# Kernel optimization log

Hardware: AMD Instinct MI355X
Metric: run time of the kernel (lower is better)

The kernel has to match this reference:

```python
import jax, jax.numpy as jnp
import numpy as np

B, H, D, N, RPE = 4, 8, 64, 4096, 64
GAMMA = 0.999
N_LAYERS = 3
EPS = 1e-5


def _layernorm(x, w, b):
    mu = jnp.mean(x, axis=-1, keepdims=True)
    var = jnp.mean((x - mu) ** 2, axis=-1, keepdims=True)
    return (x - mu) / jnp.sqrt(var + EPS) * w + b


def _rpe(pos, pp_w, pp_b, ln_w, ln_b, lw, lb, oln_w, oln_b, out_w, out_b):
    # pos: [m, 1] scalar relative positions -> [h, m, d] Toeplitz kernel values
    x = pos @ pp_w + pp_b                       # [m, rpe_dim]
    for i in range(N_LAYERS):                   # residual=False path
        x = _layernorm(x, ln_w[i], ln_b[i])
        x = jax.nn.relu(x) @ lw[i] + lb[i]
    x = jax.nn.relu(_layernorm(x, oln_w, oln_b)) @ out_w + out_b  # [m, h*d]
    m = x.shape[0]
    return x.reshape(m, H, D).transpose(1, 0, 2)  # 'n (h d) -> h n d'


def setup_inputs() -> dict:
    key = jax.random.key(0)
    ks = jax.random.split(key, 4)
    x = jax.random.normal(ks[0], (B, H, N, D), dtype=jnp.float32)
    pp_w = jax.random.normal(ks[1], (1, RPE), dtype=jnp.float32) * 0.1
    pp_b = jnp.zeros((RPE,), dtype=jnp.float32)
    ln_w = jnp.ones((N_LAYERS, RPE), dtype=jnp.float32)
    ln_b = jnp.zeros((N_LAYERS, RPE), dtype=jnp.float32)
    lw = jax.random.normal(ks[2], (N_LAYERS, RPE, RPE), dtype=jnp.float32) * 0.1
    lb = jnp.zeros((N_LAYERS, RPE), dtype=jnp.float32)
    oln_w = jnp.ones((RPE,), dtype=jnp.float32)
    oln_b = jnp.zeros((RPE,), dtype=jnp.float32)
    out_w = jax.random.normal(ks[3], (RPE, H * D), dtype=jnp.float32) * 0.1
    out_b = jnp.zeros((H * D,), dtype=jnp.float32)
    return {"x": x, "pp_w": pp_w, "pp_b": pp_b, "ln_w": ln_w, "ln_b": ln_b,
            "lw": lw, "lb": lb, "oln_w": oln_w, "oln_b": oln_b,
            "out_w": out_w, "out_b": out_b}


def reference(x, pp_w, pp_b, ln_w, ln_b, lw, lb, oln_w, oln_b, out_w, out_b):
    # Tno.forward_fft, causal=True, use_decay=True, par_type=1
    rpe_args = (pp_w, pp_b, ln_w, ln_b, lw, lb, oln_w, oln_b, out_w, out_b)
    zero = _rpe(jnp.zeros((1, 1), dtype=x.dtype), *rpe_args)          # [h,1,d]
    pos_idx = jnp.arange(1, N, dtype=x.dtype).reshape(-1, 1)          # [n-1,1]
    pos = _rpe(pos_idx, *rpe_args)                                    # [h,n-1,d]
    coef = jnp.arange(1, N, dtype=x.dtype).reshape(1, -1, 1)
    pos = (GAMMA ** coef) * pos                                       # exp decay
    a = jax.nn.silu(jnp.concatenate([zero, pos, zero], axis=1))       # [h,n+1,d]
    # causal Toeplitz conv via length-2n FFT
    y = jnp.fft.rfft(x, 2 * N, axis=-2)                               # [b,h,n+1,d] cplx
    v = jnp.fft.rfft(a, 2 * N, axis=-2)[None]                         # [1,h,n+1,d]
    out = jnp.fft.irfft(v * y, 2 * N, axis=-2)[:, :, :N, :]
    return out
```

## Files before the change

### kernel.cpp

```cpp
#include <hip/hip_runtime.h>
#include <math.h>

#define NSEQ 4096
#define MFT  4096
#define CHX  2048
#define CHA  512

#define LPAD 4224
static __device__ __forceinline__ int pad(int i) { return i + (i >> 5); }

static __device__ __forceinline__ float wsum64(float v) {
    v += __shfl_xor(v, 1);
    v += __shfl_xor(v, 2);
    v += __shfl_xor(v, 4);
    v += __shfl_xor(v, 8);
    v += __shfl_xor(v, 16);
    v += __shfl_xor(v, 32);
    return v;
}

__global__ __launch_bounds__(256) void k_twiddle(float2* __restrict__ tw) {
    int t = blockIdx.x * 256 + threadIdx.x;
    float fr = (float)t * (2.0f / (float)MFT);
    tw[t] = make_float2(cospif(fr), -sinpif(fr));
}

__global__ __launch_bounds__(256) void k_transpose(const float* __restrict__ src,
                                                   float* __restrict__ dst,
                                                   int R, int C) {
    __shared__ float tile[64][65];
    size_t slab = (size_t)blockIdx.z * (size_t)R * (size_t)C;
    int c0 = blockIdx.x * 64, r0 = blockIdx.y * 64;
    int t = threadIdx.x;
    int tc = t & 63, t4 = t >> 6;
    const float* s = src + slab + (size_t)r0 * C + c0;
#pragma unroll
    for (int k = 0; k < 16; ++k) {
        int rr = t4 + k * 4;
        tile[rr][tc] = s[(size_t)rr * C + tc];
    }
    __syncthreads();
    float* d = dst + slab + (size_t)c0 * R + r0;
#pragma unroll
    for (int k = 0; k < 16; ++k) {
        int cc = t4 + k * 4;
        d[(size_t)cc * R + tc] = tile[tc][cc];
    }
}

static __device__ __forceinline__ void ln_pair(float& x0, float& x1, float w, float b) {
    float mu0 = wsum64(x0) * (1.0f / 64.0f);
    float mu1 = wsum64(x1) * (1.0f / 64.0f);
    float d0 = x0 - mu0, d1 = x1 - mu1;
    float v0 = wsum64(d0 * d0) * (1.0f / 64.0f);
    float v1 = wsum64(d1 * d1) * (1.0f / 64.0f);
    x0 = d0 * rsqrtf(v0 + 1e-5f) * w + b;
    x1 = d1 * rsqrtf(v1 + 1e-5f) * w + b;
}

__global__ __launch_bounds__(256) void k_rpe(
    const float* __restrict__ pp_w, const float* __restrict__ pp_b,
    const float* __restrict__ ln_w, const float* __restrict__ ln_b,
    const float* __restrict__ lw,   const float* __restrict__ lb,
    const float* __restrict__ oln_w,const float* __restrict__ oln_b,
    const float* __restrict__ out_w,const float* __restrict__ out_b,
    float* __restrict__ aU)
{
    const int wave = threadIdx.x >> 6;
    const int lane = threadIdx.x & 63;
    const int mbase = (blockIdx.x * 4 + wave) * 2;
    const float m0 = (float)mbase, m1 = (float)(mbase + 1);

    float x0 = fmaf(m0, pp_w[lane], pp_b[lane]);
    float x1 = fmaf(m1, pp_w[lane], pp_b[lane]);

    for (int L = 0; L < 3; ++L) {
        ln_pair(x0, x1, ln_w[L * 64 + lane], ln_b[L * 64 + lane]);
        float r0 = fmaxf(x0, 0.0f), r1 = fmaxf(x1, 0.0f);
        float y0 = lb[L * 64 + lane], y1 = y0;
        const float* W = lw + L * 4096;
#pragma unroll 8
        for (int i = 0; i < 64; ++i) {
            float wi = W[i * 64 + lane];
            float a0 = __shfl(r0, i);
            float a1 = __shfl(r1, i);
            y0 = fmaf(a0, wi, y0);
            y1 = fmaf(a1, wi, y1);
        }
        x0 = y0; x1 = y1;
    }
    ln_pair(x0, x1, oln_w[lane], oln_b[lane]);
    float r0 = fmaxf(x0, 0.0f), r1 = fmaxf(x1, 0.0f);

    float acc0[8], acc1[8];
#pragma unroll
    for (int k = 0; k < 8; ++k) {
        float ob = out_b[k * 64 + lane];
        acc0[k] = ob; acc1[k] = ob;
    }
#pragma unroll 4
    for (int i = 0; i < 64; ++i) {
        float a0 = __shfl(r0, i);
        float a1 = __shfl(r1, i);
        const float* Wr = out_w + i * 512;
#pragma unroll
        for (int k = 0; k < 8; ++k) {
            float wv = Wr[k * 64 + lane];
            acc0[k] = fmaf(a0, wv, acc0[k]);
            acc1[k] = fmaf(a1, wv, acc1[k]);
        }
    }
    const float LOGG = -0.0010005003335835335f;
    float d0 = __expf(m0 * LOGG);
    float d1 = __expf(m1 * LOGG);
    float* row0 = aU + (size_t)mbase * 512;
    float* row1 = row0 + 512;
#pragma unroll
    for (int k = 0; k < 8; ++k) {
        int c = k * 64 + lane;
        float v0 = acc0[k] * d0; v0 = v0 / (1.0f + __expf(-v0));
        float v1 = acc1[k] * d1; v1 = v1 / (1.0f + __expf(-v1));
        row0[c] = v0;
        row1[c] = v1;
    }
}

static __device__ __forceinline__ void cmulrw(float& r, float& i, float wr, float wi) {
    float t = r * wr - i * wi;
    i = r * wi + i * wr;
    r = t;
}

template<bool INV>
static __device__ __forceinline__ void dft4(float& ar, float& ai, float& br, float& bi,
                                            float& cr, float& ci, float& dr, float& di) {
    float t0r = ar + cr, t0i = ai + ci, t1r = ar - cr, t1i = ai - ci;
    float t2r = br + dr, t2i = bi + di, t3r = br - dr, t3i = bi - di;
    float u3r = INV ? -t3i : t3i;
    float u3i = INV ?  t3r : -t3r;
    ar = t0r + t2r; ai = t0i + t2i;
    br = t1r + u3r; bi = t1i + u3i;
    cr = t0r - t2r; ci = t0i - t2i;
    dr = t1r - u3r; di = t1i - u3i;
}

template<bool INV>
static __device__ __forceinline__ void radix16(float (&vr)[16], float (&vi)[16]) {
    const float C1 = 0.92387953251128674f;
    const float S1 = 0.38268343236508978f;
    const float R2 = 0.70710678118654752f;
    const float SG = INV ? 1.0f : -1.0f;
#pragma unroll
    for (int na = 0; na < 4; ++na)
        dft4<INV>(vr[na], vi[na], vr[na + 4], vi[na + 4],
                  vr[na + 8], vi[na + 8], vr[na + 12], vi[na + 12]);
    cmulrw(vr[5],  vi[5],   C1, SG * S1);
    cmulrw(vr[9],  vi[9],   R2, SG * R2);
    cmulrw(vr[13], vi[13],  S1, SG * C1);
    cmulrw(vr[6],  vi[6],   R2, SG * R2);
    {
        float tmp = vr[10];
        if (INV) { vr[10] = -vi[10]; vi[10] =  tmp; }
        else     { vr[10] =  vi[10]; vi[10] = -tmp; }
    }
    cmulrw(vr[14], vi[14], -R2, SG * R2);
    cmulrw(vr[7],  vi[7],   S1, SG * C1);
    cmulrw(vr[11], vi[11], -R2, SG * R2);
    cmulrw(vr[15], vi[15], -C1, -SG * S1);
    float yr[16], yi[16];
#pragma unroll
    for (int kb = 0; kb < 4; ++kb) {
        float ar = vr[4*kb+0], ai = vi[4*kb+0], br = vr[4*kb+1], bi = vi[4*kb+1];
        float cr = vr[4*kb+2], ci = vi[4*kb+2], dr = vr[4*kb+3], di = vi[4*kb+3];
        dft4<INV>(ar, ai, br, bi, cr, ci, dr, di);
        yr[kb]      = ar; yi[kb]      = ai;
        yr[kb + 4]  = br; yi[kb + 4]  = bi;
        yr[kb + 8]  = cr; yi[kb + 8]  = ci;
        yr[kb + 12] = dr; yi[kb + 12] = di;
    }
#pragma unroll
    for (int k = 0; k < 16; ++k) { vr[k] = yr[k]; vi[k] = yi[k]; }
}

template<bool INV>
static __device__ __forceinline__ void fft4096_reg(float (&vr)[16], float (&vi)[16],
    float* __restrict__ lRe, float* __restrict__ lIm,
    const float2* __restrict__ tw, int t)
{
    radix16<INV>(vr, vi);
    __syncthreads();
#pragma unroll
    for (int k3 = 0; k3 < 16; ++k3) {
        int L = t + (k3 << 8);
        lRe[pad(L)] = vr[k3]; lIm[pad(L)] = vi[k3];
    }
    __syncthreads();
    {
        int n1 = t & 15, k3 = t >> 4;
        float2 w = tw[k3 << 4];
        float wim = INV ? -w.y : w.y;
        float cr = 1.0f, ci = 0.0f;
#pragma unroll
        for (int n2 = 0; n2 < 16; ++n2) {
            int L = n1 + (n2 << 4) + (k3 << 8);
            float xr = lRe[pad(L)], xi = lIm[pad(L)];
            vr[n2] = xr * cr - xi * ci;
            vi[n2] = xr * ci + xi * cr;
            float ncr = cr * w.x - ci * wim;
            ci = cr * wim + ci * w.x; cr = ncr;
        }
    }
    radix16<INV>(vr, vi);
    __syncthreads();
#pragma unroll
    for (int k2 = 0; k2 < 16; ++k2) {
        int L = t + (k2 << 8);
        lRe[pad(L)] = vr[k2]; lIm[pad(L)] = vi[k2];
    }
    __syncthreads();
    {
        float2 w = tw[t];
        float wim = INV ? -w.y : w.y;
        float cr = 1.0f, ci = 0.0f;
#pragma unroll
        for (int n1 = 0; n1 < 16; ++n1) {
            int L = (t << 4) + n1;
            float xr = lRe[pad(L)], xi = lIm[pad(L)];
            vr[n1] = xr * cr - xi * ci;
            vi[n1] = xr * ci + xi * cr;
            float ncr = cr * w.x - ci * wim;
            ci = cr * wim + ci * w.x; cr = ncr;
        }
    }
    radix16<INV>(vr, vi);
}

__global__ __launch_bounds__(256, 4) void k_fft_fwd(const float2* __restrict__ src,
                                                    float2* __restrict__ dst,
                                                    const float2* __restrict__ tw) {
    __shared__ float lRe[LPAD];
    __shared__ float lIm[LPAD];
    const int t = threadIdx.x;
    const float2* s = src + (size_t)blockIdx.x * 2048;
    float vr[16], vi[16];
#pragma unroll
    for (int n3 = 0; n3 < 8; ++n3) {
        float2 v = s[t + (n3 << 8)];
        vr[n3] = v.x; vi[n3] = v.y;
    }
#pragma unroll
    for (int n3 = 8; n3 < 16; ++n3) { vr[n3] = 0.0f; vi[n3] = 0.0f; }
    fft4096_reg<false>(vr, vi, lRe, lIm, tw, t);
    float2* d = dst + (size_t)blockIdx.x * 4096;
#pragma unroll
    for (int k1 = 0; k1 < 16; ++k1) {
        d[t + (k1 << 8)] = make_float2(vr[k1], vi[k1]);
    }
}

__global__ __launch_bounds__(256, 4) void k_fft_conv_inv(const float2* __restrict__ xrow,
                                                         const float2* __restrict__ Za,
                                                         const float2* __restrict__ tw,
                                                         float* __restrict__ yT) {
    __shared__ float lRe[LPAD];
    __shared__ float lIm[LPAD];
    const int t = threadIdx.x;
    const int bc = blockIdx.x;
    const int ca = bc & 511;
    const float2* s = xrow + (size_t)bc * 2048;
    float vr[16], vi[16];
#pragma unroll
    for (int n3 = 0; n3 < 8; ++n3) {
        float2 v = s[t + (n3 << 8)];
        vr[n3] = v.x; vi[n3] = v.y;
    }
#pragma unroll
    for (int n3 = 8; n3 < 16; ++n3) { vr[n3] = 0.0f; vi[n3] = 0.0f; }
    fft4096_reg<false>(vr, vi, lRe, lIm, tw, t);

    __syncthreads();
#pragma unroll
    for (int k1 = 0; k1 < 16; ++k1) {
        int L = t + (k1 << 8);
        lRe[pad(L)] = vr[k1]; lIm[pad(L)] = vi[k1];
    }
    __syncthreads();

    const float2* za = Za + (size_t)ca * 4096;
    for (int f = t; f <= 2048; f += 256) {
        const int fm = (4096 - f) & 4095;
        float Xfr = lRe[pad(f)],  Xfi = lIm[pad(f)];
        float Xmr = lRe[pad(fm)], Xmi = lIm[pad(fm)];
        float2 Af = za[f], Am = za[fm];
        float Exr = 0.5f * (Xfr + Xmr), Exi = 0.5f * (Xfi - Xmi);
        float Oxr = 0.5f * (Xfi + Xmi), Oxi = 0.5f * (Xmr - Xfr);
        float Ear = 0.5f * (Af.x + Am.x), Eai = 0.5f * (Af.y - Am.y);
        float Oar = 0.5f * (Af.y + Am.y), Oai = 0.5f * (Am.x - Af.x);
        float fr = (float)f * (1.0f / 4096.0f);
        float cp = cospif(fr), sp = sinpif(fr);
        float tOxr = cp * Oxr + sp * Oxi, tOxi = cp * Oxi - sp * Oxr;
        float tOar = cp * Oar + sp * Oai, tOai = cp * Oai - sp * Oar;
        float Xpr = Exr + tOxr, Xpi = Exi + tOxi;
        float Xqr = Exr - tOxr, Xqi = Exi - tOxi;
        float Apr = Ear + tOar, Api = Eai + tOai;
        float Aqr = Ear - tOar, Aqi = Eai - tOai;
        float Pr = Xpr * Apr - Xpi * Api, Pi = Xpr * Api + Xpi * Apr;
        float Qr = Xqr * Aqr - Xqi * Aqi, Qi = Xqr * Aqi + Xqi * Aqr;
        float Sr = 0.5f * (Pr + Qr), Si = 0.5f * (Pi + Qi);
        float Dr = 0.5f * (Pr - Qr), Di = 0.5f * (Pi - Qi);
        float Cr = cp * Dr - sp * Di, Ci = cp * Di + sp * Dr;
        lRe[pad(f)]  = Sr - Ci;  lIm[pad(f)]  = Si + Cr;
        lRe[pad(fm)] = Sr + Ci;  lIm[pad(fm)] = Cr - Si;
    }
    __syncthreads();
#pragma unroll
    for (int n3 = 0; n3 < 16; ++n3) {
        int L = t + (n3 << 8);
        vr[n3] = lRe[pad(L)]; vi[n3] = lIm[pad(L)];
    }
    fft4096_reg<true>(vr, vi, lRe, lIm, tw, t);

    const float sc = 1.0f / 4096.0f;
    float2* dst = (float2*)yT + (size_t)bc * 2048;
#pragma unroll
    for (int k1 = 0; k1 < 8; ++k1) {
        int idx = t + (k1 << 8);
        dst[idx] = make_float2(vr[k1] * sc, vi[k1] * sc);
    }
}

extern "C" void kernel_launch(void* const* d_in, const int* in_sizes, int n_in,
                              void* d_out, int out_size, void* d_ws, size_t ws_size,
                              hipStream_t stream) {
    const float* x     = (const float*)d_in[0];
    const float* pp_w  = (const float*)d_in[1];
    const float* pp_b  = (const float*)d_in[2];
    const float* ln_w  = (const float*)d_in[3];
    const float* ln_b  = (const float*)d_in[4];
    const float* lw    = (const float*)d_in[5];
    const float* lb    = (const float*)d_in[6];
    const float* oln_w = (const float*)d_in[7];
    const float* oln_b = (const float*)d_in[8];
    const float* out_w = (const float*)d_in[9];
    const float* out_b = (const float*)d_in[10];
    float* out = (float*)d_out;
    char* ws = (char*)d_ws;

    float2* tw = (float2*)(ws);
    float*  xT = (float*)(ws + 65536u);
    float*  aU = (float*)(ws + 65536u + 33554432u);
    float*  aT = (float*)(ws + 65536u + 33554432u + 8388608u);
    float2* Za = (float2*)(ws + 65536u + 33554432u + 16777216u);
    float*  yT = xT;

    k_twiddle<<<16, 256, 0, stream>>>(tw);
    k_transpose<<<dim3(1, 64, 32), 256, 0, stream>>>(x, xT, 4096, 64);
    k_rpe<<<512, 256, 0, stream>>>(pp_w, pp_b, ln_w, ln_b, lw, lb,
                                   oln_w, oln_b, out_w, out_b, aU);
    k_transpose<<<dim3(8, 64, 1), 256, 0, stream>>>(aU, aT, 4096, 512);
    k_fft_fwd<<<CHA, 256, 0, stream>>>((const float2*)aT, Za, tw);
    k_fft_conv_inv<<<CHX, 256, 0, stream>>>((const float2*)xT, Za, tw, yT);
    k_transpose<<<dim3(64, 1, 32), 256, 0, stream>>>(yT, out, 64, 4096);
}
```

Before: 181.4 us.

## Fuse x transpose and RPE MLP into one prologue kernel, inline FFT twiddles

Merges the x transpose and the RPE MLP into one launch split by block index. The MLP now processes four positions per wave and writes its output directly in transposed layout with float4 stores, which removes the intermediate aU buffer and its transpose kernel. The twiddle-table kernel is dropped in favour of computing cos/sin per thread inside the FFT, and shared memory moves from split real/imag arrays to interleaved float2. Together these cut launches and global traffic, at the cost of extra transcendental work and more register pressure in the MLP path.

```diff
diff --git a/kernel.cpp b/kernel.cpp
--- a/kernel.cpp
+++ b/kernel.cpp
@@ -6,8 +6,8 @@
 #define CHX  2048
 #define CHA  512
 
-#define LPAD 4224
-static __device__ __forceinline__ int pad(int i) { return i + (i >> 5); }
+#define LP2 4224
+static __device__ __forceinline__ int pf(int i) { return i + (i >> 5); }
 
 static __device__ __forceinline__ float wsum64(float v) {
     v += __shfl_xor(v, 1);
@@ -19,10 +19,122 @@
     return v;
 }
 
-__global__ __launch_bounds__(256) void k_twiddle(float2* __restrict__ tw) {
-    int t = blockIdx.x * 256 + threadIdx.x;
-    float fr = (float)t * (2.0f / (float)MFT);
-    tw[t] = make_float2(cospif(fr), -sinpif(fr));
+static __device__ __forceinline__ void ln1(float& x, float w, float b) {
+    float mu = wsum64(x) * (1.0f / 64.0f);
+    float d = x - mu;
+    float v = wsum64(d * d) * (1.0f / 64.0f);
+    x = d * rsqrtf(v + 1e-5f) * w + b;
+}
+
+__global__ __launch_bounds__(256) void k_pre(
+    const float* __restrict__ x,
+    const float* __restrict__ pp_w, const float* __restrict__ pp_b,
+    const float* __restrict__ ln_w, const float* __restrict__ ln_b,
+    const float* __restrict__ lw,   const float* __restrict__ lb,
+    const float* __restrict__ oln_w,const float* __restrict__ oln_b,
+    const float* __restrict__ out_w,const float* __restrict__ out_b,
+    float* __restrict__ xT, float* __restrict__ aT)
+{
+    __shared__ float tile[64][65];
+    const int t = threadIdx.x;
+
+    if (blockIdx.x < 2048) {
+        const int slab = blockIdx.x >> 6;
+        const int r0 = (blockIdx.x & 63) * 64;
+        const size_t base = (size_t)slab * 262144u;
+        const int tc = t & 63, t4 = t >> 6;
+        const float* s = x + base + (size_t)r0 * 64;
+#pragma unroll
+        for (int k = 0; k < 16; ++k) {
+            int rr = t4 + k * 4;
+            tile[rr][tc] = s[rr * 64 + tc];
+        }
+        __syncthreads();
+        float* d = xT + base + r0;
+#pragma unroll
+        for (int k = 0; k < 16; ++k) {
+            int cc = t4 + k * 4;
+            d[(size_t)cc * 4096 + tc] = tile[tc][cc];
+        }
+        return;
+    }
+
+    const int wave = t >> 6;
+    const int lane = t & 63;
+    const int mbase = ((int)(blockIdx.x - 2048) * 4 + wave) * 4;
+
+    float mm[4], xx[4];
+#pragma unroll
+    for (int p = 0; p < 4; ++p) {
+        mm[p] = (float)(mbase + p);
+        xx[p] = fmaf(mm[p], pp_w[lane], pp_b[lane]);
+    }
+
+    for (int L = 0; L < 3; ++L) {
+        float w = ln_w[L * 64 + lane], b = ln_b[L * 64 + lane];
+        float r[4], y[4];
+#pragma unroll
+        for (int p = 0; p < 4; ++p) {
+            ln1(xx[p], w, b);
+            r[p] = fmaxf(xx[p], 0.0f);
+            y[p] = lb[L * 64 + lane];
+        }
+        const float* W = lw + L * 4096;
+#pragma unroll 8
+        for (int i = 0; i < 64; ++i) {
+            float wi = W[i * 64 + lane];
+#pragma unroll
+            for (int p = 0; p < 4; ++p)
+                y[p] = fmaf(__shfl(r[p], i), wi, y[p]);
+        }
+#pragma unroll
+        for (int p = 0; p < 4; ++p) xx[p] = y[p];
+    }
+    {
+        float w = oln_w[lane], b = oln_b[lane];
+#pragma unroll
+        for (int p = 0; p < 4; ++p) {
+            ln1(xx[p], w, b);
+            xx[p] = fmaxf(xx[p], 0.0f);
+        }
+    }
+
+    float acc[4][8];
+#pragma unroll
+    for (int k = 0; k < 8; ++k) {
+        float ob = out_b[k * 64 + lane];
+#pragma unroll
+        for (int p = 0; p < 4; ++p) acc[p][k] = ob;
+    }
+#pragma unroll 4
+    for (int i = 0; i < 64; ++i) {
+        float a0 = __shfl(xx[0], i), a1 = __shfl(xx[1], i);
+        float a2 = __shfl(xx[2], i), a3 = __shfl(xx[3], i);
+        const float* Wr = out_w + i * 512;
+#pragma unroll
+        for (int k = 0; k < 8; ++k) {
+            float wv = Wr[k * 64 + lane];
+            acc[0][k] = fmaf(a0, wv, acc[0][k]);
+            acc[1][k] = fmaf(a1, wv, acc[1][k]);
+            acc[2][k] = fmaf(a2, wv, acc[2][k]);
+            acc[3][k] = fmaf(a3, wv, acc[3][k]);
+        }
+    }
+    const float LOGG = -0.0010005003335835335f;
+    float dy[4];
+#pragma unroll
+    for (int p = 0; p < 4; ++p) dy[p] = __expf(mm[p] * LOGG);
+#pragma unroll
+    for (int k = 0; k < 8; ++k) {
+        int c = k * 64 + lane;
+        float4 o;
+        float v;
+        v = acc[0][k] * dy[0]; o.x = v / (1.0f + __expf(-v));
+        v = acc[1][k] * dy[1]; o.y = v / (1.0f + __expf(-v));
+        v = acc[2][k] * dy[2]; o.z = v / (1.0f + __expf(-v));
+        v = acc[3][k] * dy[3]; o.w = v / (1.0f + __expf(-v));
+        *(float4*)(aT + (size_t)c * 4096 + mbase) = o;
+    }
 }
 
 __global__ __launch_bounds__(256) void k_transpose(const float* __restrict__ src,
@@ -45,83 +157,6 @@
     for (int k = 0; k < 16; ++k) {
         int cc = t4 + k * 4;
         d[(size_t)cc * R + tc] = tile[tc][cc];
-    }
-}
-
-static __device__ __forceinline__ void ln_pair(float& x0, float& x1, float w, float b) {
-    float mu0 = wsum64(x0) * (1.0f / 64.0f);
-    float mu1 = wsum64(x1) * (1.0f / 64.0f);
-    float d0 = x0 - mu0, d1 = x1 - mu1;
-    float v0 = wsum64(d0 * d0) * (1.0f / 64.0f);
-    float v1 = wsum64(d1 * d1) * (1.0f / 64.0f);
-    x0 = d0 * rsqrtf(v0 + 1e-5f) * w + b;
-    x1 = d1 * rsqrtf(v1 + 1e-5f) * w + b;
-}
-
-__global__ __launch_bounds__(256) void k_rpe(
-    const float* __restrict__ pp_w, const float* __restrict__ pp_b,
-    const float* __restrict__ ln_w, const float* __restrict__ ln_b,
-    const float* __restrict__ lw,   const float* __restrict__ lb,
-    const float* __restrict__ oln_w,const float* __restrict__ oln_b,
-    const float* __restrict__ out_w,const float* __restrict__ out_b,
-    float* __restrict__ aU)
-{
-    const int wave = threadIdx.x >> 6;
-    const int lane = threadIdx.x & 63;
-    const int mbase = (blockIdx.x * 4 + wave) * 2;
-    const float m0 = (float)mbase, m1 = (float)(mbase + 1);
-
-    float x0 = fmaf(m0, pp_w[lane], pp_b[lane]);
-    float x1 = fmaf(m1, pp_w[lane], pp_b[lane]);
-
-    for (int L = 0; L < 3; ++L) {
-        ln_pair(x0, x1, ln_w[L * 64 + lane], ln_b[L * 64 + lane]);
-        float r0 = fmaxf(x0, 0.0f), r1 = fmaxf(x1, 0.0f);
-        float y0 = lb[L * 64 + lane], y1 = y0;
-        const float* W = lw + L * 4096;
-#pragma unroll 8
-        for (int i = 0; i < 64; ++i) {
-            float wi = W[i * 64 + lane];
-            float a0 = __shfl(r0, i);
-            float a1 = __shfl(r1, i);
-            y0 = fmaf(a0, wi, y0);
-            y1 = fmaf(a1, wi, y1);
-        }
-        x0 = y0; x1 = y1;
-    }
-    ln_pair(x0, x1, oln_w[lane], oln_b[lane]);
-    float r0 = fmaxf(x0, 0.0f), r1 = fmaxf(x1, 0.0f);
-
-    float acc0[8], acc1[8];
-#pragma unroll
-    for (int k = 0; k < 8; ++k) {
-        float ob = out_b[k * 64 + lane];
-        acc0[k] = ob; acc1[k] = ob;
-    }
-#pragma unroll 4
-    for (int i = 0; i < 64; ++i) {
-        float a0 = __shfl(r0, i);
-        float a1 = __shfl(r1, i);
-        const float* Wr = out_w + i * 512;
-#pragma unroll
-        for (int k = 0; k < 8; ++k) {
-            float wv = Wr[k * 64 + lane];
-            acc0[k] = fmaf(a0, wv, acc0[k]);
-            acc1[k] = fmaf(a1, wv, acc1[k]);
-        }
-    }
-    const float LOGG = -0.0010005003335835335f;
-    float d0 = __expf(m0 * LOGG);
-    float d1 = __expf(m1 * LOGG);
-    float* row0 = aU + (size_t)mbase * 512;
-    float* row1 = row0 + 512;
-#pragma unroll
-    for (int k = 0; k < 8; ++k) {
-        int c = k * 64 + lane;
-        float v0 = acc0[k] * d0; v0 = v0 / (1.0f + __expf(-v0));
-        float v1 = acc1[k] * d1; v1 = v1 / (1.0f + __expf(-v1));
-        row0[c] = v0;
-        row1[c] = v1;
     }
 }
 
@@ -184,62 +219,55 @@
 
 template<bool INV>
 static __device__ __forceinline__ void fft4096_reg(float (&vr)[16], float (&vi)[16],
-    float* __restrict__ lRe, float* __restrict__ lIm,
-    const float2* __restrict__ tw, int t)
+                                                   float2* __restrict__ lds, int t)
 {
     radix16<INV>(vr, vi);
     __syncthreads();
 #pragma unroll
-    for (int k3 = 0; k3 < 16; ++k3) {
-        int L = t + (k3 << 8);
-        lRe[pad(L)] = vr[k3]; lIm[pad(L)] = vi[k3];
-    }
+    for (int k3 = 0; k3 < 16; ++k3)
+        lds[pf(t + (k3 << 8))] = make_float2(vr[k3], vi[k3]);
     __syncthreads();
     {
         int n1 = t & 15, k3 = t >> 4;
-        float2 w = tw[k3 << 4];
-        float wim = INV ? -w.y : w.y;
+        float ang = (float)k3 * (1.0f / 128.0f);
+        float wr = cospif(ang);
+        float wi = INV ? sinpif(ang) : -sinpif(ang);
         float cr = 1.0f, ci = 0.0f;
 #pragma unroll
         for (int n2 = 0; n2 < 16; ++n2) {
-            int L = n1 + (n2 << 4) + (k3 << 8);
-            float xr = lRe[pad(L)], xi = lIm[pad(L)];
-            vr[n2] = xr * cr - xi * ci;
-            vi[n2] = xr * ci + xi * cr;
-            float ncr = cr * w.x - ci * wim;
-            ci = cr * wim + ci * w.x; cr = ncr;
+            float2 v = lds[pf(n1 + (n2 << 4) + (k3 << 8))];
+            vr[n2] = v.x * cr - v.y * ci;
+            vi[n2] = v.x * ci + v.y * cr;
+            float ncr = cr * wr - ci * wi;
+            ci = cr * wi + ci * wr; cr = ncr;
         }
     }
     radix16<INV>(vr, vi);
     __syncthreads();
 #pragma unroll
-    for (int k2 = 0; k2 < 16; ++k2) {
-        int L = t + (k2 << 8);
-        lRe[pad(L)] = vr[k2]; lIm[pad(L)] = vi[k2];
-    }
+    for (int k2 = 0; k2 < 16; ++k2)
+        lds[pf(t + (k2 << 8))] = make_float2(vr[k2], vi[k2]);
     __syncthreads();
     {
-        float2 w = tw[t];
-        float wim = INV ? -w.y : w.y;
+        float ang = (float)t * (1.0f / 2048.0f);
+        float wr = cospif(ang);
+        float wi = INV ? sinpif(ang) : -sinpif(ang);
         float cr = 1.0f, ci = 0.0f;
 #pragma unroll
         for (int n1 = 0; n1 < 16; ++n1) {
-            int L = (t << 4) + n1;
-            float xr = lRe[pad(L)], xi = lIm[pad(L)];
-            vr[n1] = xr * cr - xi * ci;
-            vi[n1] = xr * ci + xi * cr;
-            float ncr = cr * w.x - ci * wim;
-            ci = cr * wim + ci * w.x; cr = ncr;
+            float2 v = lds[pf((t << 4) + n1)];
+            vr[n1] = v.x * cr - v.y * ci;
+            vi[n1] = v.x * ci + v.y * cr;
+            float ncr = cr * wr - ci * wi;
+            ci = cr * wi + ci * wr; cr = ncr;
         }
     }
     radix16<INV>(vr, vi);
 }
 
 __global__ __launch_bounds__(256, 4) void k_fft_fwd(const float2* __restrict__ src,
-                                                    float2* __restrict__ dst,
-                                                    const float2* __restrict__ tw) {
-    __shared__ float lRe[LPAD];
-    __shared__ float lIm[LPAD];
+                                                    float2* __restrict__ dst) {
+    __shared__ float2 lds[LP2];
     const int t = threadIdx.x;
     const float2* s = src + (size_t)blockIdx.x * 2048;
     float vr[16], vi[16];
@@ -250,20 +278,17 @@
     }
 #pragma unroll
     for (int n3 = 8; n3 < 16; ++n3) { vr[n3] = 0.0f; vi[n3] = 0.0f; }
-    fft4096_reg<false>(vr, vi, lRe, lIm, tw, t);
+    fft4096_reg<false>(vr, vi, lds, t);
     float2* d = dst + (size_t)blockIdx.x * 4096;
 #pragma unroll
-    for (int k1 = 0; k1 < 16; ++k1) {
+    for (int k1 = 0; k1 < 16; ++k1)
         d[t + (k1 << 8)] = make_float2(vr[k1], vi[k1]);
-    }
 }
 
 __global__ __launch_bounds__(256, 4) void k_fft_conv_inv(const float2* __restrict__ xrow,
                                                          const float2* __restrict__ Za,
-                                                         const float2* __restrict__ tw,
                                                          float* __restrict__ yT) {
-    __shared__ float lRe[LPAD];
-    __shared__ float lIm[LPAD];
+    __shared__ float2 lds[LP2];
     const int t = threadIdx.x;
     const int bc = blockIdx.x;
     const int ca = bc & 511;
@@ -276,24 +301,21 @@
     }
 #pragma unroll
     for (int n3 = 8; n3 < 16; ++n3) { vr[n3] = 0.0f; vi[n3] = 0.0f; }
-    fft4096_reg<false>(vr, vi, lRe, lIm, tw, t);
-
-    __syncthreads();
-#pragma unroll
-    for (int k1 = 0; k1 < 16; ++k1) {
-        int L = t + (k1 << 8);
-        lRe[pad(L)] = vr[k1]; lIm[pad(L)] = vi[k1];
-    }
+    fft4096_reg<false>(vr, vi, lds, t);
+
+    __syncthreads();
+#pragma unroll
+    for (int k1 = 0; k1 < 16; ++k1)
+        lds[pf(t + (k1 << 8))] = make_float2(vr[k1], vi[k1]);
     __syncthreads();
 
     const float2* za = Za + (size_t)ca * 4096;
     for (int f = t; f <= 2048; f += 256) {
         const int fm = (4096 - f) & 4095;
-        float Xfr = lRe[pad(f)],  Xfi = lIm[pad(f)];
-        float Xmr = lRe[pad(fm)], Xmi = lIm[pad(fm)];
+        float2 Xf = lds[pf(f)], Xm = lds[pf(fm)];
         float2 Af = za[f], Am = za[fm];
-        float Exr = 0.5f * (Xfr + Xmr), Exi = 0.5f * (Xfi - Xmi);
-        float Oxr = 0.5f * (Xfi + Xmi), Oxi = 0.5f * (Xmr - Xfr);
+        float Exr = 0.5f * (Xf.x + Xm.x), Exi = 0.5f * (Xf.y - Xm.y);
+        float Oxr = 0.5f * (Xf.y + Xm.y), Oxi = 0.5f * (Xm.x - Xf.x);
         float Ear = 0.5f * (Af.x + Am.x), Eai = 0.5f * (Af.y - Am.y);
         float Oar = 0.5f * (Af.y + Am.y), Oai = 0.5f * (Am.x - Af.x);
         float fr = (float)f * (1.0f / 4096.0f);
@@ -309,16 +331,16 @@
         float Sr = 0.5f * (Pr + Qr), Si = 0.5f * (Pi + Qi);
         float Dr = 0.5f * (Pr - Qr), Di = 0.5f * (Pi - Qi);
         float Cr = cp * Dr - sp * Di, Ci = cp * Di + sp * Dr;
-        lRe[pad(f)]  = Sr - Ci;  lIm[pad(f)]  = Si + Cr;
-        lRe[pad(fm)] = Sr + Ci;  lIm[pad(fm)] = Cr - Si;
+        lds[pf(f)]  = make_float2(Sr - Ci, Si + Cr);
+        lds[pf(fm)] = make_float2(Sr + Ci, Cr - Si);
     }
     __syncthreads();
 #pragma unroll
     for (int n3 = 0; n3 < 16; ++n3) {
-        int L = t + (n3 << 8);
-        vr[n3] = lRe[pad(L)]; vi[n3] = lIm[pad(L)];
-    }
-    fft4096_reg<true>(vr, vi, lRe, lIm, tw, t);
+        float2 v = lds[pf(t + (n3 << 8))];
+        vr[n3] = v.x; vi[n3] = v.y;
+    }
+    fft4096_reg<true>(vr, vi, lds, t);
 
     const float sc = 1.0f / 4096.0f;
     float2* dst = (float2*)yT + (size_t)bc * 2048;
@@ -346,19 +368,14 @@
     float* out = (float*)d_out;
     char* ws = (char*)d_ws;
 
-    float2* tw = (float2*)(ws);
-    float*  xT = (float*)(ws + 65536u);
-    float*  aU = (float*)(ws + 65536u + 33554432u);
-    float*  aT = (float*)(ws + 65536u + 33554432u + 8388608u);
-    float2* Za = (float2*)(ws + 65536u + 33554432u + 16777216u);
+    float*  xT = (float*)(ws);
+    float*  aT = (float*)(ws + 33554432u);
+    float2* Za = (float2*)(ws + 41943040u);
     float*  yT = xT;
 
-    k_twiddle<<<16, 256, 0, stream>>>(tw);
-    k_transpose<<<dim3(1, 64, 32), 256, 0, stream>>>(x, xT, 4096, 64);
-    k_rpe<<<512, 256, 0, stream>>>(pp_w, pp_b, ln_w, ln_b, lw, lb,
-                                   oln_w, oln_b, out_w, out_b, aU);
-    k_transpose<<<dim3(8, 64, 1), 256, 0, stream>>>(aU, aT, 4096, 512);
-    k_fft_fwd<<<CHA, 256, 0, stream>>>((const float2*)aT, Za, tw);
-    k_fft_conv_inv<<<CHX, 256, 0, stream>>>((const float2*)xT, Za, tw, yT);
+    k_pre<<<2304, 256, 0, stream>>>(x, pp_w, pp_b, ln_w, ln_b, lw, lb,
+                                    oln_w, oln_b, out_w, out_b, xT, aT);
+    k_fft_fwd<<<CHA, 256, 0, stream>>>((const float2*)aT, Za);
+    k_fft_conv_inv<<<CHX, 256, 0, stream>>>((const float2*)xT, Za, yT);
     k_transpose<<<dim3(64, 1, 32), 256, 0, stream>>>(yT, out, 64, 4096);
 }
```

New measurement: 192.3 us. 1.06x slower.
